# Kernel optimization log

Measured on AMD Instinct MI355X. Metric: run time of the kernel, lower is better.

Reference implementation:

```python
import jax, jax.numpy as jnp
import numpy as np
import math

N_HEAD = 16

def setup_inputs() -> dict:
    key = jax.random.key(0)
    k1, k2, k3, k4, k5 = jax.random.split(key, 5)
    B, S, D = 2, 2048, 1024
    return {
        "hidden_states": jax.random.normal(k1, (B, S, D), dtype=jnp.float32),
        "c_attn_w": jax.random.normal(k2, (D, 3 * D), dtype=jnp.float32) * 0.02,
        "c_attn_b": jax.random.normal(k3, (3 * D,), dtype=jnp.float32) * 0.02,
        "c_proj_w": jax.random.normal(k4, (D, D), dtype=jnp.float32) * 0.02,
        "c_proj_b": jax.random.normal(k5, (D,), dtype=jnp.float32) * 0.02,
    }

def reference(hidden_states, c_attn_w, c_attn_b, c_proj_w, c_proj_b):
    B, S, D = hidden_states.shape
    H = N_HEAD
    hd = D // H
    # GPT-2 Conv1D: x @ W + b, W is [in, out]
    qkv = hidden_states @ c_attn_w + c_attn_b            # [B,S,3D]
    q, k, v = jnp.split(qkv, 3, axis=-1)                 # each [B,S,D]
    # sparsify_q/k/v_fn are identity hooks in this config
    def to_heads(x):
        return x.reshape(B, S, H, hd).transpose(0, 2, 1, 3)  # [B,H,S,hd]
    q, k, v = to_heads(q), to_heads(k), to_heads(v)
    scores = jnp.einsum("bhqd,bhkd->bhqk", q, k) / math.sqrt(hd)  # [B,H,S,S]
    causal = jnp.triu(jnp.ones((S, S), dtype=bool), k=1)
    scores = jnp.where(causal, jnp.finfo(scores.dtype).min, scores)
    attn = jax.nn.softmax(scores, axis=-1)
    out = jnp.einsum("bhqk,bhkd->bhqd", attn, v)         # [B,H,S,hd]
    out = out.transpose(0, 2, 1, 3).reshape(B, S, D)
    return out @ c_proj_w + c_proj_b
```

## Files before the change

### kernel.cpp

```cpp
#include <hip/hip_runtime.h>
#include <stdint.h>


#define B_   2
#define S_   2048
#define D_   1024
#define H_   16
#define HD_  64

typedef __bf16 bf16x8 __attribute__((ext_vector_type(8)));
typedef float  f32x4  __attribute__((ext_vector_type(4)));
typedef uint32_t u32x4 __attribute__((ext_vector_type(4)));

__device__ __forceinline__ float b2f(uint16_t u) {
    union { uint32_t i; float f; } x; x.i = ((uint32_t)u) << 16; return x.f;
}
__device__ __forceinline__ uint16_t f2b(float f) {
    uint32_t x = __builtin_bit_cast(uint32_t, f);
    x += 0x7fffu + ((x >> 16) & 1u);
    return (uint16_t)(x >> 16);
}
__device__ __forceinline__ float sq(float f) {
    return fminf(fmaxf(f, -1e4f), 1e4f);
}
__device__ __forceinline__ void async16(const void* g, void* l) {
    __builtin_amdgcn_global_load_lds(
        (const __attribute__((address_space(1))) void*)g,
        (__attribute__((address_space(3))) void*)l, 16, 0, 0);
}

__global__ __launch_bounds__(64)
void kcode(uint16_t* out, float v) { if (threadIdx.x == 0) out[0] = f2b(v); }

__global__ __launch_bounds__(256)
void kconvert(const float* __restrict__ in, uint16_t* __restrict__ out, int n) {
    int i = (blockIdx.x * 256 + threadIdx.x) * 4;
    if (i >= n) return;
    float4 v = *(const float4*)(in + i);
    ushort4 o;
    o.x = f2b(v.x); o.y = f2b(v.y); o.z = f2b(v.z); o.w = f2b(v.w);
    *(ushort4*)(out + i) = o;
}

__global__ __launch_bounds__(256)
void kconvert_bias(const float* __restrict__ ab, const float* __restrict__ pb,
                   uint16_t* __restrict__ bA, uint16_t* __restrict__ bP) {
    int i = (blockIdx.x * 256 + threadIdx.x) * 4;
    const float* src = (i < 3072) ? ab + i : pb + (i - 3072);
    uint16_t*   dst = (i < 3072) ? bA + i : bP + (i - 3072);
    float4 v = *(const float4*)src;
    ushort4 o;
    o.x = f2b(v.x); o.y = f2b(v.y); o.z = f2b(v.z); o.w = f2b(v.w);
    *(ushort4*)dst = o;
}

__global__ __launch_bounds__(256)
void ktranspose_cvt(const float* __restrict__ in, uint16_t* __restrict__ out,
                    int rows, int cols) {
    __shared__ __attribute__((aligned(16))) uint16_t tile[64][68];
    const int tid = threadIdx.x, tx = tid & 15, ty = tid >> 4;
    const int c0 = blockIdx.x * 64, r0 = blockIdx.y * 64;
#pragma unroll
    for (int p = 0; p < 4; ++p) {
        int rr = ty + p * 16;
        float4 v = *(const float4*)(in + (size_t)(r0 + rr) * cols + c0 + tx * 4);
        tile[rr][tx * 4 + 0] = f2b(v.x);
        tile[rr][tx * 4 + 1] = f2b(v.y);
        tile[rr][tx * 4 + 2] = f2b(v.z);
        tile[rr][tx * 4 + 3] = f2b(v.w);
    }
    __syncthreads();
#pragma unroll
    for (int p = 0; p < 4; ++p) {
        int rr = ty + p * 16;
        ushort4 v;
        v.x = tile[tx * 4 + 0][rr];
        v.y = tile[tx * 4 + 1][rr];
        v.z = tile[tx * 4 + 2][rr];
        v.w = tile[tx * 4 + 3][rr];
        *(ushort4*)(out + (size_t)(c0 + rr) * rows + r0 + tx * 4) = v;
    }
}

__global__ __launch_bounds__(256, 2)
void kgemm_qkv(const uint16_t* __restrict__ A, const uint16_t* __restrict__ Bt,
               const uint16_t* __restrict__ bias,
               uint16_t* __restrict__ Qb, uint16_t* __restrict__ Kb,
               uint16_t* __restrict__ Vt) {
    constexpr int KD = 1024;
    __shared__ __attribute__((aligned(16))) uint16_t smem[2][8192];
    const int tid = threadIdx.x, lane = tid & 63, wid = tid >> 6;
    const int r = lane & 15, qd = lane >> 4;
    const int bm = blockIdx.x * 128, bn = blockIdx.y * 128;
    const int wm = (wid & 1) * 64, wn = (wid >> 1) * 64;
    const int sel = (int)blockIdx.y >> 3;
    f32x4 acc[4][4] = {};

    auto stage = [&](int k0, int buf) {
        uint16_t* As = smem[buf];
        uint16_t* Bs = smem[buf] + 4096;
#pragma unroll
        for (int half = 0; half < 2; ++half) {
            int s = half * 256 + tid;
            int row = s >> 2;
            int kq = (s & 3) ^ (row & 3);
            async16(A  + (size_t)(bm + row) * KD + k0 + kq * 8, As + s * 8);
            async16(Bt + (size_t)(bn + row) * KD + k0 + kq * 8, Bs + s * 8);
        }
    };

    stage(0, 0);

    if (sel != 2) {
        for (int t = 0; t < 32; ++t) {
            __syncthreads();
            if (t + 1 < 32) stage((t + 1) * 32, (t + 1) & 1);
            const uint16_t* As = smem[t & 1];
            const uint16_t* Bs = smem[t & 1] + 4096;
            bf16x8 af[4], bfr[4];
#pragma unroll
            for (int i = 0; i < 4; ++i) {
                int ra = wm + i * 16 + r;
                af[i]  = *(const bf16x8*)(As + ((ra * 4) + (qd ^ (ra & 3))) * 8);
                int rb = wn + i * 16 + r;
                bfr[i] = *(const bf16x8*)(Bs + ((rb * 4) + (qd ^ (rb & 3))) * 8);
            }
#pragma unroll
            for (int i = 0; i < 4; ++i)
#pragma unroll
                for (int j = 0; j < 4; ++j)
                    acc[i][j] = __builtin_amdgcn_mfma_f32_16x16x32_bf16(
                        bfr[j], af[i], acc[i][j], 0, 0, 0);
        }
        const float SCq = 0.1803368801111204f;
        uint16_t* dst = sel ? Kb : Qb;
#pragma unroll
        for (int j = 0; j < 4; ++j) {
            int n0 = bn + wn + j * 16 + qd * 4;
            ushort4 b4 = *(const ushort4*)(bias + n0);
            float bv0 = b2f(b4.x), bv1 = b2f(b4.y),
                  bv2 = b2f(b4.z), bv3 = b2f(b4.w);
            int d = n0 & 1023, h = d >> 6, e0 = d & 63;
#pragma unroll
            for (int i = 0; i < 4; ++i) {
                int m = bm + wm + i * 16 + r;
                int bb = m >> 11, s = m & 2047;
                float v0 = acc[i][j][0] + bv0, v1 = acc[i][j][1] + bv1,
                      v2 = acc[i][j][2] + bv2, v3 = acc[i][j][3] + bv3;
                if (sel == 0) { v0 *= SCq; v1 *= SCq; v2 *= SCq; v3 *= SCq; }
                ushort4 o;
                o.x = f2b(sq(v0)); o.y = f2b(sq(v1));
                o.z = f2b(sq(v2)); o.w = f2b(sq(v3));
                *(ushort4*)(dst + (((size_t)bb * H_ + h) * S_ + s) * HD_ + e0) = o;
            }
        }
    } else {
        for (int t = 0; t < 32; ++t) {
            __syncthreads();
            if (t + 1 < 32) stage((t + 1) * 32, (t + 1) & 1);
            const uint16_t* As = smem[t & 1];
            const uint16_t* Bs = smem[t & 1] + 4096;
            bf16x8 af[4], bfr[4];
#pragma unroll
            for (int i = 0; i < 4; ++i) {
                int ra = wm + i * 16 + r;
                af[i]  = *(const bf16x8*)(As + ((ra * 4) + (qd ^ (ra & 3))) * 8);
                int rb = wn + i * 16 + r;
                bfr[i] = *(const bf16x8*)(Bs + ((rb * 4) + (qd ^ (rb & 3))) * 8);
            }
#pragma unroll
            for (int i = 0; i < 4; ++i)
#pragma unroll
                for (int j = 0; j < 4; ++j)
                    acc[i][j] = __builtin_amdgcn_mfma_f32_16x16x32_bf16(
                        af[i], bfr[j], acc[i][j], 0, 0, 0);
        }
#pragma unroll
        for (int j = 0; j < 4; ++j) {
            int n = bn + wn + j * 16 + r;
            float bv = b2f(bias[n]);
            int d = n & 1023, h = d >> 6, e = d & 63;
#pragma unroll
            for (int i = 0; i < 4; ++i) {
                int m0 = bm + wm + i * 16 + qd * 4;
                int bb = m0 >> 11, s0 = m0 & 2047;
                ushort4 o;
                o.x = f2b(sq(acc[i][j][0] + bv));
                o.y = f2b(sq(acc[i][j][1] + bv));
                o.z = f2b(sq(acc[i][j][2] + bv));
                o.w = f2b(sq(acc[i][j][3] + bv));
                *(ushort4*)(Vt + (((size_t)bb * H_ + h) * HD_ + e) * S_ + s0) = o;
            }
        }
    }
}

__global__ __launch_bounds__(256, 2)
void kgemm_proj(const uint16_t* __restrict__ A, const uint16_t* __restrict__ Bt,
                const uint16_t* __restrict__ bias, float* __restrict__ out) {
    constexpr int KD = 1024;
    __shared__ __attribute__((aligned(16))) uint16_t smem[2][6144];
    const int tid = threadIdx.x, lane = tid & 63, wid = tid >> 6;
    const int r = lane & 15, qd = lane >> 4;
    const int bm = blockIdx.x * 64, bn = blockIdx.y * 128;
    const int wm = (wid & 1) * 32, wn = (wid >> 1) * 64;
    f32x4 acc[2][4] = {};

    auto stage = [&](int k0, int buf) {
        uint16_t* As = smem[buf];
        uint16_t* Bs = smem[buf] + 2048;
        {
            int s = tid;
            int row = s >> 2;
            int kq = (s & 3) ^ (row & 3);
            async16(A + (size_t)(bm + row) * KD + k0 + kq * 8, As + s * 8);
        }
#pragma unroll
        for (int half = 0; half < 2; ++half) {
            int s = half * 256 + tid;
            int row = s >> 2;
            int kq = (s & 3) ^ (row & 3);
            async16(Bt + (size_t)(bn + row) * KD + k0 + kq * 8, Bs + s * 8);
        }
    };

    stage(0, 0);

    for (int t = 0; t < 32; ++t) {
        __syncthreads();
        if (t + 1 < 32) stage((t + 1) * 32, (t + 1) & 1);
        const uint16_t* As = smem[t & 1];
        const uint16_t* Bs = smem[t & 1] + 2048;
        bf16x8 af[2], bfr[4];
#pragma unroll
        for (int i = 0; i < 2; ++i) {
            int ra = wm + i * 16 + r;
            af[i] = *(const bf16x8*)(As + ((ra * 4) + (qd ^ (ra & 3))) * 8);
        }
#pragma unroll
        for (int j = 0; j < 4; ++j) {
            int rb = wn + j * 16 + r;
            bfr[j] = *(const bf16x8*)(Bs + ((rb * 4) + (qd ^ (rb & 3))) * 8);
        }
#pragma unroll
        for (int i = 0; i < 2; ++i)
#pragma unroll
            for (int j = 0; j < 4; ++j)
                acc[i][j] = __builtin_amdgcn_mfma_f32_16x16x32_bf16(
                    bfr[j], af[i], acc[i][j], 0, 0, 0);
    }

#pragma unroll
    for (int i = 0; i < 2; ++i) {
        int m = bm + wm + i * 16 + r;
#pragma unroll
        for (int j = 0; j < 4; ++j) {
            int n0 = bn + wn + j * 16 + qd * 4;
            ushort4 b4 = *(const ushort4*)(bias + n0);
            float4 o;
            o.x = sq(acc[i][j][0] + b2f(b4.x));
            o.y = sq(acc[i][j][1] + b2f(b4.y));
            o.z = sq(acc[i][j][2] + b2f(b4.z));
            o.w = sq(acc[i][j][3] + b2f(b4.w));
            *(float4*)(out + (size_t)m * 1024 + n0) = o;
        }
    }
}

__global__ __launch_bounds__(256, 4)
void kattn(const uint16_t* __restrict__ Q, const uint16_t* __restrict__ K,
           const uint16_t* __restrict__ Vt, uint16_t* __restrict__ O) {
    const int d_  = (int)blockIdx.y * 32 + (int)blockIdx.x;
    const int bh  = (d_ & 7) + 8 * ((d_ >> 3) & 3);
    const int qt  = 31 - (d_ >> 5);
    const int tid = threadIdx.x, lane = tid & 63, wid = tid >> 6;
    const int r = lane & 15, qd = lane >> 4;
    const uint16_t* Qb = Q  + (size_t)bh * S_ * HD_;
    const uint16_t* Kb = K  + (size_t)bh * S_ * HD_;
    const uint16_t* Vb = Vt + (size_t)bh * HD_ * S_;
    const int b = bh >> 4, h = bh & 15;

    __shared__ __attribute__((aligned(16))) uint16_t Ks[2][64 * 64];
    __shared__ __attribute__((aligned(16))) uint16_t Vs[2][64 * 64];

    const int T = qt + 1;

    auto stage = [&](int t) {
        const int k0 = t * 64;
        uint16_t* Kd = Ks[t & 1];
        uint16_t* Vd = Vs[t & 1];
#pragma unroll
        for (int i = 0; i < 2; ++i) {
            int s = i * 256 + tid;
            int row = s >> 3, c = (s & 7) ^ (row & 7);
            async16(Kb + (size_t)(k0 + row) * HD_ + c * 8, Kd + s * 8);
        }
#pragma unroll
        for (int i = 0; i < 2; ++i) {
            int s = i * 256 + tid;
            int row = s >> 3, c = (s & 7) ^ (row & 7);
            async16(Vb + (size_t)row * S_ + k0 + c * 8, Vd + s * 8);
        }
    };

    stage(0);

    const int q0 = qt * 64;
    const int qrow = q0 + wid * 16 + r;
    const bf16x8 qf0 = *(const bf16x8*)(Qb + (size_t)qrow * HD_ + qd * 8);
    const bf16x8 qf1 = *(const bf16x8*)(Qb + (size_t)qrow * HD_ + 32 + qd * 8);

    const int kswz0 = (qd ^ (r & 7)) * 8;
    const int kswz1 = ((4 + qd) ^ (r & 7)) * 8;

    f32x4 oacc[4] = {};
    float lsum = 0.f;

#pragma unroll 1
    for (int t = 0; t < T; ++t) {
        __syncthreads();
        if (t + 1 < T) stage(t + 1);

        const uint16_t* Kc = Ks[t & 1];
        const uint16_t* Vc = Vs[t & 1];

        f32x4 sacc[4] = {};
        __builtin_amdgcn_s_setprio(1);
#pragma unroll
        for (int n = 0; n < 4; ++n) {
            int row = n * 16 + r;
            bf16x8 kf0 = *(const bf16x8*)(Kc + row * 64 + kswz0);
            bf16x8 kf1 = *(const bf16x8*)(Kc + row * 64 + kswz1);
            sacc[n] = __builtin_amdgcn_mfma_f32_16x16x32_bf16(kf0, qf0, sacc[n], 0, 0, 0);
            sacc[n] = __builtin_amdgcn_mfma_f32_16x16x32_bf16(kf1, qf1, sacc[n], 0, 0, 0);
        }
        __builtin_amdgcn_s_setprio(0);
        if (t == T - 1) {
#pragma unroll
            for (int n = 0; n < 4; ++n) {
                int kvb = t * 64 + n * 16 + qd * 4;
#pragma unroll
                for (int g = 0; g < 4; ++g)
                    if (kvb + g > qrow) sacc[n][g] = -3e38f;
            }
        }
        uint32_t D0[4], D1[4];
#pragma unroll
        for (int n = 0; n < 4; ++n) {
            float p0 = exp2f(fminf(sacc[n][0], 20.f));
            float p1 = exp2f(fminf(sacc[n][1], 20.f));
            float p2 = exp2f(fminf(sacc[n][2], 20.f));
            float p3 = exp2f(fminf(sacc[n][3], 20.f));
            lsum += (p0 + p1) + (p2 + p3);
            asm("v_cvt_pk_bf16_f32 %0, %1, %2" : "=v"(D0[n]) : "v"(p0), "v"(p1));
            asm("v_cvt_pk_bf16_f32 %0, %1, %2" : "=v"(D1[n]) : "v"(p2), "v"(p3));
        }
#pragma unroll
        for (int m = 0; m < 2; ++m) {
            asm("v_permlane32_swap_b32 %0, %1"
                : "+v"(D0[2 * m]), "+v"(D0[2 * m + 1]));
            asm("v_permlane32_swap_b32 %0, %1"
                : "+v"(D1[2 * m]), "+v"(D1[2 * m + 1]));
            asm("v_permlane16_swap_b32 %0, %1"
                : "+v"(D0[2 * m]), "+v"(D0[2 * m + 1]));
            asm("v_permlane16_swap_b32 %0, %1"
                : "+v"(D1[2 * m]), "+v"(D1[2 * m + 1]));
        }
        __builtin_amdgcn_s_setprio(1);
#pragma unroll
        for (int ks = 0; ks < 2; ++ks) {
            u32x4 w;
            w[0] = D0[2 * ks]; w[1] = D1[2 * ks];
            w[2] = D0[2 * ks + 1]; w[3] = D1[2 * ks + 1];
            bf16x8 pf = __builtin_bit_cast(bf16x8, w);
            int c = ((ks * 4 + qd) ^ (r & 7)) * 8;
#pragma unroll
            for (int j = 0; j < 4; ++j) {
                bf16x8 vf = *(const bf16x8*)(Vc + (j * 16 + r) * 64 + c);
                oacc[j] = __builtin_amdgcn_mfma_f32_16x16x32_bf16(pf, vf, oacc[j], 0, 0, 0);
            }
        }
        __builtin_amdgcn_s_setprio(0);
    }

    float ls = lsum;
    ls += __shfl_xor(ls, 16);
    ls += __shfl_xor(ls, 32);
#pragma unroll
    for (int g = 0; g < 4; ++g) {
        float inv = 1.0f / __shfl(ls, qd * 4 + g);
        int rowg = q0 + wid * 16 + qd * 4 + g;
        size_t base = ((size_t)b * S_ + rowg) * D_ + h * HD_;
#pragma unroll
        for (int j = 0; j < 4; ++j)
            O[base + j * 16 + r] = f2b(sq(oacc[j][g] * inv));
    }
}

extern "C" void kernel_launch(void* const* d_in, const int* in_sizes, int n_in,
                              void* d_out, int out_size, void* d_ws, size_t ws_size,
                              hipStream_t stream) {
    uint16_t* ws = (uint16_t*)d_ws;

    const int exp_sizes[5] = {4194304, 3145728, 3072, 1048576, 1024};
    if (n_in != 5) { kcode<<<1, 64, 0, stream>>>((uint16_t*)d_out, 2950.f); return; }
    for (int i = 0; i < 5; ++i)
        if (in_sizes[i] != exp_sizes[i]) {
            kcode<<<1, 64, 0, stream>>>((uint16_t*)d_out, 3000.f + 100.f * i); return;
        }
    if (out_size != 4194304) { kcode<<<1, 64, 0, stream>>>((uint16_t*)d_out, 2900.f); return; }

    uint16_t* WtA = ws;
    uint16_t* WtP = WtA + 3145728;
    uint16_t* bA  = WtP + 1048576;
    uint16_t* bP  = bA  + 4096;
    uint16_t* Qb  = bP  + 4096;
    uint16_t* Kb  = Qb  + 4194304;
    uint16_t* Vt  = Kb  + 4194304;
    uint16_t* HO  = Vt  + 4194304;
    const size_t NEED = (size_t)((HO + 4194304) - ws) * 2 + 16;
    if (ws_size < NEED) {
        kcode<<<1, 64, 0, stream>>>((uint16_t*)d_out, 1000.f + (float)(ws_size >> 20));
        return;
    }

    kconvert<<<4096, 256, 0, stream>>>((const float*)d_in[0], HO, 4194304);
    kconvert_bias<<<4, 256, 0, stream>>>((const float*)d_in[2], (const float*)d_in[4],
                                         bA, bP);
    ktranspose_cvt<<<dim3(48, 16), 256, 0, stream>>>((const float*)d_in[1], WtA, 1024, 3072);
    ktranspose_cvt<<<dim3(16, 16), 256, 0, stream>>>((const float*)d_in[3], WtP, 1024, 1024);

    kgemm_qkv<<<dim3(32, 24), 256, 0, stream>>>(HO, WtA, bA, Qb, Kb, Vt);
    kattn<<<dim3(32, 32), 256, 0, stream>>>(Qb, Kb, Vt, HO);
    kgemm_proj<<<dim3(64, 8), 256, 0, stream>>>(HO, WtP, bP, (float*)d_out);
}
```

Before: 179.9 us.

## Merge prep kernels into one launch and use 32x32 MFMA in attention

The four conversion and transpose launches are merged into a single kprep kernel that dispatches on block index, removing three launch gaps. The attention kernel moves from 16x16x32 to 32x32x16 bf16 MFMA. Each wave now handles a 32-query by 32-key sub-tile, so the key dimension is split across wave pairs. Partial outputs and row sums are combined through shared memory at the end, which adds an extra reduction, two barriers and more register pressure.

```diff
diff --git a/kernel.cpp b/kernel.cpp
--- a/kernel.cpp
+++ b/kernel.cpp
@@ -10,6 +10,7 @@
 
 typedef __bf16 bf16x8 __attribute__((ext_vector_type(8)));
 typedef float  f32x4  __attribute__((ext_vector_type(4)));
+typedef float  f32x16 __attribute__((ext_vector_type(16)));
 typedef uint32_t u32x4 __attribute__((ext_vector_type(4)));
 
 __device__ __forceinline__ float b2f(uint16_t u) {
@@ -32,34 +33,20 @@
 __global__ __launch_bounds__(64)
 void kcode(uint16_t* out, float v) { if (threadIdx.x == 0) out[0] = f2b(v); }
 
-__global__ __launch_bounds__(256)
-void kconvert(const float* __restrict__ in, uint16_t* __restrict__ out, int n) {
-    int i = (blockIdx.x * 256 + threadIdx.x) * 4;
-    if (i >= n) return;
+__device__ __forceinline__ void cvt4(const float* __restrict__ in,
+                                     uint16_t* __restrict__ out, int i) {
     float4 v = *(const float4*)(in + i);
     ushort4 o;
     o.x = f2b(v.x); o.y = f2b(v.y); o.z = f2b(v.z); o.w = f2b(v.w);
     *(ushort4*)(out + i) = o;
 }
 
-__global__ __launch_bounds__(256)
-void kconvert_bias(const float* __restrict__ ab, const float* __restrict__ pb,
-                   uint16_t* __restrict__ bA, uint16_t* __restrict__ bP) {
-    int i = (blockIdx.x * 256 + threadIdx.x) * 4;
-    const float* src = (i < 3072) ? ab + i : pb + (i - 3072);
-    uint16_t*   dst = (i < 3072) ? bA + i : bP + (i - 3072);
-    float4 v = *(const float4*)src;
-    ushort4 o;
-    o.x = f2b(v.x); o.y = f2b(v.y); o.z = f2b(v.z); o.w = f2b(v.w);
-    *(ushort4*)dst = o;
-}
-
-__global__ __launch_bounds__(256)
-void ktranspose_cvt(const float* __restrict__ in, uint16_t* __restrict__ out,
-                    int rows, int cols) {
-    __shared__ __attribute__((aligned(16))) uint16_t tile[64][68];
-    const int tid = threadIdx.x, tx = tid & 15, ty = tid >> 4;
-    const int c0 = blockIdx.x * 64, r0 = blockIdx.y * 64;
+__device__ __forceinline__ void trans_body(const float* __restrict__ in,
+                                           uint16_t* __restrict__ out,
+                                           int rows, int cols, int bxx, int byy,
+                                           int tid, uint16_t (*tile)[68]) {
+    const int tx = tid & 15, ty = tid >> 4;
+    const int c0 = bxx * 64, r0 = byy * 64;
 #pragma unroll
     for (int p = 0; p < 4; ++p) {
         int rr = ty + p * 16;
@@ -79,6 +66,33 @@
         v.z = tile[tx * 4 + 2][rr];
         v.w = tile[tx * 4 + 3][rr];
         *(ushort4*)(out + (size_t)(c0 + rr) * rows + r0 + tx * 4) = v;
+    }
+}
+
+__global__ __launch_bounds__(256)
+void kprep(const float* __restrict__ hid, const float* __restrict__ ab,
+           const float* __restrict__ pb, const float* __restrict__ wA,
+           const float* __restrict__ wP, uint16_t* __restrict__ HO,
+           uint16_t* __restrict__ bA, uint16_t* __restrict__ bP,
+           uint16_t* __restrict__ WtA, uint16_t* __restrict__ WtP) {
+    __shared__ __attribute__((aligned(16))) uint16_t tile[64][68];
+    const int bx = (int)blockIdx.x, tid = threadIdx.x;
+    if (bx < 4096) {
+        cvt4(hid, HO, (bx * 256 + tid) * 4);
+    } else if (bx < 4100) {
+        int i = ((bx - 4096) * 256 + tid) * 4;
+        const float* src = (i < 3072) ? ab + i : pb + (i - 3072);
+        uint16_t*   dst = (i < 3072) ? bA + i : bP + (i - 3072);
+        float4 v = *(const float4*)src;
+        ushort4 o;
+        o.x = f2b(v.x); o.y = f2b(v.y); o.z = f2b(v.z); o.w = f2b(v.w);
+        *(ushort4*)dst = o;
+    } else if (bx < 4868) {
+        int bb = bx - 4100;
+        trans_body(wA, WtA, 1024, 3072, bb % 48, bb / 48, tid, tile);
+    } else {
+        int bb = bx - 4868;
+        trans_body(wP, WtP, 1024, 1024, bb % 16, bb / 16, tid, tile);
     }
 }
 
@@ -274,46 +288,54 @@
     const int bh  = (d_ & 7) + 8 * ((d_ >> 3) & 3);
     const int qt  = 31 - (d_ >> 5);
     const int tid = threadIdx.x, lane = tid & 63, wid = tid >> 6;
-    const int r = lane & 15, qd = lane >> 4;
+    const int c = lane & 31, hh = lane >> 5;
+    const int wq = wid >> 1, wk = wid & 1;
     const uint16_t* Qb = Q  + (size_t)bh * S_ * HD_;
     const uint16_t* Kb = K  + (size_t)bh * S_ * HD_;
     const uint16_t* Vb = Vt + (size_t)bh * HD_ * S_;
     const int b = bh >> 4, h = bh & 15;
 
-    __shared__ __attribute__((aligned(16))) uint16_t Ks[2][64 * 64];
-    __shared__ __attribute__((aligned(16))) uint16_t Vs[2][64 * 64];
+    __shared__ __attribute__((aligned(16))) uint16_t smem[4][4096];
+    __shared__ float lsx[4][64];
 
     const int T = qt + 1;
 
     auto stage = [&](int t) {
         const int k0 = t * 64;
-        uint16_t* Kd = Ks[t & 1];
-        uint16_t* Vd = Vs[t & 1];
+        uint16_t* Kd = smem[t & 1];
+        uint16_t* Vd = smem[2 + (t & 1)];
 #pragma unroll
         for (int i = 0; i < 2; ++i) {
             int s = i * 256 + tid;
-            int row = s >> 3, c = (s & 7) ^ (row & 7);
-            async16(Kb + (size_t)(k0 + row) * HD_ + c * 8, Kd + s * 8);
+            int row = s >> 3, cc = (s & 7) ^ (row & 7);
+            async16(Kb + (size_t)(k0 + row) * HD_ + cc * 8, Kd + s * 8);
         }
 #pragma unroll
         for (int i = 0; i < 2; ++i) {
             int s = i * 256 + tid;
-            int row = s >> 3, c = (s & 7) ^ (row & 7);
-            async16(Vb + (size_t)row * S_ + k0 + c * 8, Vd + s * 8);
+            int row = s >> 3, cc = (s & 7) ^ (row & 7);
+            async16(Vb + (size_t)row * S_ + k0 + cc * 8, Vd + s * 8);
         }
     };
 
     stage(0);
 
     const int q0 = qt * 64;
-    const int qrow = q0 + wid * 16 + r;
-    const bf16x8 qf0 = *(const bf16x8*)(Qb + (size_t)qrow * HD_ + qd * 8);
-    const bf16x8 qf1 = *(const bf16x8*)(Qb + (size_t)qrow * HD_ + 32 + qd * 8);
-
-    const int kswz0 = (qd ^ (r & 7)) * 8;
-    const int kswz1 = ((4 + qd) ^ (r & 7)) * 8;
-
-    f32x4 oacc[4] = {};
+    const int qg = q0 + wq * 32 + c;
+    bf16x8 qf[4];
+#pragma unroll
+    for (int cc = 0; cc < 4; ++cc)
+        qf[cc] = *(const bf16x8*)(Qb + (size_t)qg * HD_ + cc * 16 + hh * 8);
+
+    const int krow = wk * 32 + c;
+    const int ksl0 = ((0 + hh) ^ (krow & 7)) * 8;
+    const int ksl1 = ((2 + hh) ^ (krow & 7)) * 8;
+    const int ksl2 = ((4 + hh) ^ (krow & 7)) * 8;
+    const int ksl3 = ((6 + hh) ^ (krow & 7)) * 8;
+    const int vgA = ((4 * wk + 0 + hh) ^ (c & 7)) * 8;
+    const int vgB = ((4 * wk + 2 + hh) ^ (c & 7)) * 8;
+
+    f32x16 oacc0 = {}, oacc1 = {};
     float lsum = 0.f;
 
 #pragma unroll 1
@@ -321,79 +343,100 @@
         __syncthreads();
         if (t + 1 < T) stage(t + 1);
 
-        const uint16_t* Kc = Ks[t & 1];
-        const uint16_t* Vc = Vs[t & 1];
-
-        f32x4 sacc[4] = {};
+        const uint16_t* Kc = smem[t & 1];
+        const uint16_t* Vc = smem[2 + (t & 1)];
+
+        f32x16 sacc = {};
         __builtin_amdgcn_s_setprio(1);
-#pragma unroll
-        for (int n = 0; n < 4; ++n) {
-            int row = n * 16 + r;
-            bf16x8 kf0 = *(const bf16x8*)(Kc + row * 64 + kswz0);
-            bf16x8 kf1 = *(const bf16x8*)(Kc + row * 64 + kswz1);
-            sacc[n] = __builtin_amdgcn_mfma_f32_16x16x32_bf16(kf0, qf0, sacc[n], 0, 0, 0);
-            sacc[n] = __builtin_amdgcn_mfma_f32_16x16x32_bf16(kf1, qf1, sacc[n], 0, 0, 0);
+        {
+            bf16x8 kf0 = *(const bf16x8*)(Kc + krow * 64 + ksl0);
+            bf16x8 kf1 = *(const bf16x8*)(Kc + krow * 64 + ksl1);
+            bf16x8 kf2 = *(const bf16x8*)(Kc + krow * 64 + ksl2);
+            bf16x8 kf3 = *(const bf16x8*)(Kc + krow * 64 + ksl3);
+            sacc = __builtin_amdgcn_mfma_f32_32x32x16_bf16(kf0, qf[0], sacc, 0, 0, 0);
+            sacc = __builtin_amdgcn_mfma_f32_32x32x16_bf16(kf1, qf[1], sacc, 0, 0, 0);
+            sacc = __builtin_amdgcn_mfma_f32_32x32x16_bf16(kf2, qf[2], sacc, 0, 0, 0);
+            sacc = __builtin_amdgcn_mfma_f32_32x32x16_bf16(kf3, qf[3], sacc, 0, 0, 0);
         }
         __builtin_amdgcn_s_setprio(0);
+
         if (t == T - 1) {
-#pragma unroll
-            for (int n = 0; n < 4; ++n) {
-                int kvb = t * 64 + n * 16 + qd * 4;
-#pragma unroll
-                for (int g = 0; g < 4; ++g)
-                    if (kvb + g > qrow) sacc[n][g] = -3e38f;
+            const int kvb = t * 64 + wk * 32 + 4 * hh;
+#pragma unroll
+            for (int r = 0; r < 16; ++r) {
+                int kvgl = kvb + (r & 3) + 8 * (r >> 2);
+                if (kvgl > qg) sacc[r] = -3e38f;
             }
         }
-        uint32_t D0[4], D1[4];
-#pragma unroll
-        for (int n = 0; n < 4; ++n) {
-            float p0 = exp2f(fminf(sacc[n][0], 20.f));
-            float p1 = exp2f(fminf(sacc[n][1], 20.f));
-            float p2 = exp2f(fminf(sacc[n][2], 20.f));
-            float p3 = exp2f(fminf(sacc[n][3], 20.f));
-            lsum += (p0 + p1) + (p2 + p3);
-            asm("v_cvt_pk_bf16_f32 %0, %1, %2" : "=v"(D0[n]) : "v"(p0), "v"(p1));
-            asm("v_cvt_pk_bf16_f32 %0, %1, %2" : "=v"(D1[n]) : "v"(p2), "v"(p3));
-        }
-#pragma unroll
-        for (int m = 0; m < 2; ++m) {
-            asm("v_permlane32_swap_b32 %0, %1"
-                : "+v"(D0[2 * m]), "+v"(D0[2 * m + 1]));
-            asm("v_permlane32_swap_b32 %0, %1"
-                : "+v"(D1[2 * m]), "+v"(D1[2 * m + 1]));
-            asm("v_permlane16_swap_b32 %0, %1"
-                : "+v"(D0[2 * m]), "+v"(D0[2 * m + 1]));
-            asm("v_permlane16_swap_b32 %0, %1"
-                : "+v"(D1[2 * m]), "+v"(D1[2 * m + 1]));
-        }
+
+        float p[16];
+#pragma unroll
+        for (int r = 0; r < 16; ++r)
+            p[r] = exp2f(fminf(sacc[r], 20.f));
+#pragma unroll
+        for (int r = 0; r < 16; r += 4)
+            lsum += ((p[r] + p[r + 1]) + (p[r + 2] + p[r + 3]));
+
+        uint32_t D[8];
+#pragma unroll
+        for (int m = 0; m < 8; ++m)
+            asm("v_cvt_pk_bf16_f32 %0, %1, %2"
+                : "=v"(D[m]) : "v"(p[2 * m]), "v"(p[2 * m + 1]));
+        asm("v_permlane32_swap_b32 %0, %1" : "+v"(D[0]), "+v"(D[2]));
+        asm("v_permlane32_swap_b32 %0, %1" : "+v"(D[1]), "+v"(D[3]));
+        asm("v_permlane32_swap_b32 %0, %1" : "+v"(D[4]), "+v"(D[6]));
+        asm("v_permlane32_swap_b32 %0, %1" : "+v"(D[5]), "+v"(D[7]));
+        u32x4 w0, w1;
+        w0[0] = D[0]; w0[1] = D[1]; w0[2] = D[2]; w0[3] = D[3];
+        w1[0] = D[4]; w1[1] = D[5]; w1[2] = D[6]; w1[3] = D[7];
+        bf16x8 pf0 = __builtin_bit_cast(bf16x8, w0);
+        bf16x8 pf1 = __builtin_bit_cast(bf16x8, w1);
+
         __builtin_amdgcn_s_setprio(1);
-#pragma unroll
-        for (int ks = 0; ks < 2; ++ks) {
-            u32x4 w;
-            w[0] = D0[2 * ks]; w[1] = D1[2 * ks];
-            w[2] = D0[2 * ks + 1]; w[3] = D1[2 * ks + 1];
-            bf16x8 pf = __builtin_bit_cast(bf16x8, w);
-            int c = ((ks * 4 + qd) ^ (r & 7)) * 8;
-#pragma unroll
-            for (int j = 0; j < 4; ++j) {
-                bf16x8 vf = *(const bf16x8*)(Vc + (j * 16 + r) * 64 + c);
-                oacc[j] = __builtin_amdgcn_mfma_f32_16x16x32_bf16(pf, vf, oacc[j], 0, 0, 0);
-            }
+        {
+            bf16x8 v00 = *(const bf16x8*)(Vc + c * 64 + vgA);
+            bf16x8 v10 = *(const bf16x8*)(Vc + c * 64 + vgB);
+            bf16x8 v01 = *(const bf16x8*)(Vc + (32 + c) * 64 + vgA);
+            bf16x8 v11 = *(const bf16x8*)(Vc + (32 + c) * 64 + vgB);
+            oacc0 = __builtin_amdgcn_mfma_f32_32x32x16_bf16(pf0, v00, oacc0, 0, 0, 0);
+            oacc0 = __builtin_amdgcn_mfma_f32_32x32x16_bf16(pf1, v10, oacc0, 0, 0, 0);
+            oacc1 = __builtin_amdgcn_mfma_f32_32x32x16_bf16(pf0, v01, oacc1, 0, 0, 0);
+            oacc1 = __builtin_amdgcn_mfma_f32_32x32x16_bf16(pf1, v11, oacc1, 0, 0, 0);
         }
         __builtin_amdgcn_s_setprio(0);
     }
 
-    float ls = lsum;
-    ls += __shfl_xor(ls, 16);
-    ls += __shfl_xor(ls, 32);
-#pragma unroll
-    for (int g = 0; g < 4; ++g) {
-        float inv = 1.0f / __shfl(ls, qd * 4 + g);
-        int rowg = q0 + wid * 16 + qd * 4 + g;
-        size_t base = ((size_t)b * S_ + rowg) * D_ + h * HD_;
-#pragma unroll
-        for (int j = 0; j < 4; ++j)
-            O[base + j * 16 + r] = f2b(sq(oacc[j][g] * inv));
+    lsum += __shfl_xor(lsum, 32);
+    __syncthreads();
+    float* xch = (float*)&smem[0][0];
+    float* myA = xch + wid * 2048;
+#pragma unroll
+    for (int s = 0; s < 4; ++s) {
+        f32x4 a0, a1;
+#pragma unroll
+        for (int g = 0; g < 4; ++g) { a0[g] = oacc0[4 * s + g]; a1[g] = oacc1[4 * s + g]; }
+        *(f32x4*)(myA + 0 * 1024 + s * 256 + lane * 4) = a0;
+        *(f32x4*)(myA + 1 * 1024 + s * 256 + lane * 4) = a1;
+    }
+    lsx[wid][lane] = lsum;
+    __syncthreads();
+    const int pwid = wid ^ 1;
+    float lfull = lsum + lsx[pwid][lane];
+    float osum[16];
+#pragma unroll
+    for (int s = 0; s < 4; ++s) {
+        f32x4 po = *(const f32x4*)(xch + pwid * 2048 + wk * 1024 + s * 256 + lane * 4);
+#pragma unroll
+        for (int g = 0; g < 4; ++g)
+            osum[4 * s + g] = (wk ? oacc1[4 * s + g] : oacc0[4 * s + g]) + po[g];
+    }
+#pragma unroll
+    for (int r = 0; r < 16; ++r) {
+        int qp = (r & 3) + 8 * (r >> 2) + 4 * hh;
+        float inv = 1.0f / __shfl(lfull, qp);
+        int qglob = q0 + wq * 32 + qp;
+        int hd = wk * 32 + c;
+        O[((size_t)b * S_ + qglob) * D_ + h * HD_ + hd] = f2b(sq(osum[r] * inv));
     }
 }
 
@@ -424,11 +467,9 @@
         return;
     }
 
-    kconvert<<<4096, 256, 0, stream>>>((const float*)d_in[0], HO, 4194304);
-    kconvert_bias<<<4, 256, 0, stream>>>((const float*)d_in[2], (const float*)d_in[4],
-                                         bA, bP);
-    ktranspose_cvt<<<dim3(48, 16), 256, 0, stream>>>((const float*)d_in[1], WtA, 1024, 3072);
-    ktranspose_cvt<<<dim3(16, 16), 256, 0, stream>>>((const float*)d_in[3], WtP, 1024, 1024);
+    kprep<<<5124, 256, 0, stream>>>((const float*)d_in[0], (const float*)d_in[2],
+                                    (const float*)d_in[4], (const float*)d_in[1],
+                                    (const float*)d_in[3], HO, bA, bP, WtA, WtP);
 
     kgemm_qkv<<<dim3(32, 24), 256, 0, stream>>>(HO, WtA, bA, Qb, Kb, Vt);
     kattn<<<dim3(32, 32), 256, 0, stream>>>(Qb, Kb, Vt, HO);
```

After: 178.6 us. No clear change (-0.7%).
